# Performance work log

Hardware: AMD Instinct MI355X
Metric: run time of the kernel (lower is better)

Reference implementation:

```python
import jax, jax.numpy as jnp
import numpy as np

VOCAB = 32000
D_MODEL = 1024


def setup_inputs() -> dict:
    key = jax.random.key(0)
    k = jax.random.split(key, 8)
    B, H, T, S = 8, 16, 128, 512
    src = jax.random.randint(k[0], (B, S), 0, VOCAB)
    decode_output = jax.random.normal(k[1], (B, T, D_MODEL), dtype=jnp.float32)
    decode_attn = jax.random.uniform(k[2], (B, H, T, S), dtype=jnp.float32)
    memory = jax.random.normal(k[3], (B, S, D_MODEL), dtype=jnp.float32)
    W_gen = jax.random.normal(k[4], (VOCAB, D_MODEL), dtype=jnp.float32) * (1.0 / np.sqrt(D_MODEL))
    b_gen = jnp.zeros((VOCAB,), dtype=jnp.float32)
    W_prob = jax.random.normal(k[5], (1, 2 * D_MODEL), dtype=jnp.float32) * (1.0 / np.sqrt(2 * D_MODEL))
    b_prob = jnp.zeros((1,), dtype=jnp.float32)
    return {"src": src, "decode_output": decode_output, "decode_attn": decode_attn,
            "memory": memory, "W_gen": W_gen, "b_gen": b_gen,
            "W_prob": W_prob, "b_prob": b_prob}


def reference(src, decode_output, decode_attn, memory, W_gen, b_gen, W_prob, b_prob):
    # mean over heads: [B, T, S]
    attn = jnp.mean(decode_attn, axis=1)
    B, T, S = attn.shape
    V = W_gen.shape[0]

    # generation logits: [B, T, V]
    gen_logits = jnp.einsum('btd,vd->btv', decode_output, W_gen) + b_gen

    # context vector: [B, T, D]
    context = jnp.einsum('bts,bsd->btd', attn, memory)

    # scatter-add copy distribution over vocab: [B, T, V]
    src_exp = jnp.broadcast_to(src[:, None, :], (B, T, S))  # token ids per step
    b_idx = jnp.arange(B)[:, None, None]
    t_idx = jnp.arange(T)[None, :, None]
    copy_logits = jnp.zeros((B, T, V), dtype=attn.dtype).at[b_idx, t_idx, src_exp].add(attn)

    # copy gate: sigmoid(Linear([context; decode_output])) -> [B, T, 1]
    cat = jnp.concatenate([context, decode_output], axis=-1)
    prob = jax.nn.sigmoid(jnp.einsum('btd,od->bto', cat, W_prob) + b_prob)

    gen_p = prob * jax.nn.softmax(gen_logits, axis=-1)
    copy_p = (1.0 - prob) * jax.nn.softmax(copy_logits, axis=-1)
    final = gen_p + copy_p
    return jnp.log(final).reshape(-1, V)
```

## Files before the change

### kernel.cpp

```cpp
#include <hip/hip_runtime.h>
#include <hip/hip_bf16.h>
#include <cstddef>
#include <cstdint>

#define BB 8
#define HH 16
#define TT 128
#define SS 512
#define DD 1024
#define VV 32000
#define MM (BB * TT)

typedef float f32x4 __attribute__((ext_vector_type(4)));
typedef short short8v __attribute__((ext_vector_type(8)));
typedef unsigned short ushort8v __attribute__((ext_vector_type(8)));

__device__ __forceinline__ unsigned short f2bf(float x) {
    __hip_bfloat16 h = __float2bfloat16(x);
    return __builtin_bit_cast(unsigned short, h);
}
__device__ __forceinline__ float bf2f(unsigned short u) {
    unsigned int x = ((unsigned int)u) << 16;
    return __builtin_bit_cast(float, x);
}

__device__ __forceinline__ float wave_sum(float v) {
#pragma unroll
    for (int o = 1; o < 64; o <<= 1) v += __shfl_xor(v, o);
    return v;
}
__device__ __forceinline__ float wave_max(float v) {
#pragma unroll
    for (int o = 1; o < 64; o <<= 1) v = fmaxf(v, __shfl_xor(v, o));
    return v;
}
__device__ __forceinline__ float block_sum(float v, float* red, int tid) {
    v = wave_sum(v);
    __syncthreads();
    if ((tid & 63) == 0) red[tid >> 6] = v;
    __syncthreads();
    return red[0] + red[1] + red[2] + red[3];
}
__device__ __forceinline__ float block_max(float v, float* red, int tid) {
    v = wave_max(v);
    __syncthreads();
    if ((tid & 63) == 0) red[tid >> 6] = v;
    __syncthreads();
    return fmaxf(fmaxf(red[0], red[1]), fmaxf(red[2], red[3]));
}

__global__ void k_pm_init(int* pos_map, float* zg) {
    int i = blockIdx.x * 256 + threadIdx.x;
    if (i < BB * VV) pos_map[i] = 0x7fffffff;
    if (i < MM) zg[i] = 0.0f;
}

__global__ void k_pm_build(const int* __restrict__ src, int* pos_map) {
    int b = blockIdx.x, s = threadIdx.x;
    int tok = src[b * SS + s];
    atomicMin(&pos_map[b * VV + tok], s);
}

__global__ __launch_bounds__(256) void k_cast(const float* __restrict__ in,
                                              unsigned short* __restrict__ outp, int n8) {
    int stride = gridDim.x * 256;
    for (int i = blockIdx.x * 256 + threadIdx.x; i < n8; i += stride) {
        const float4* p = reinterpret_cast<const float4*>(in + (size_t)i * 8);
        float4 a = p[0], b = p[1];
        ushort8v u;
        u[0] = f2bf(a.x); u[1] = f2bf(a.y); u[2] = f2bf(a.z); u[3] = f2bf(a.w);
        u[4] = f2bf(b.x); u[5] = f2bf(b.y); u[6] = f2bf(b.z); u[7] = f2bf(b.w);
        *reinterpret_cast<ushort8v*>(outp + (size_t)i * 8) = u;
    }
}

__global__ __launch_bounds__(256) void k_vecdots(const float* __restrict__ memory,
                                                 const float* __restrict__ dec,
                                                 const float* __restrict__ wprob,
                                                 float* mw, float* dw) {
    int row = blockIdx.x * 4 + (threadIdx.x >> 6);
    int lane = threadIdx.x & 63;
    const float4* srcv;
    const float4* wv;
    if (row < BB * SS) {
        srcv = reinterpret_cast<const float4*>(memory + (size_t)row * DD);
        wv = reinterpret_cast<const float4*>(wprob);
    } else {
        srcv = reinterpret_cast<const float4*>(dec + (size_t)(row - BB * SS) * DD);
        wv = reinterpret_cast<const float4*>(wprob + DD);
    }
    float sum = 0.f;
#pragma unroll
    for (int k = 0; k < 4; ++k) {
        int idx = lane + 64 * k;
        float4 a = srcv[idx];
        float4 w = wv[idx];
        sum += a.x * w.x + a.y * w.y + a.z * w.z + a.w * w.w;
    }
    sum = wave_sum(sum);
    if (lane == 0) {
        if (row < BB * SS) mw[row] = sum;
        else dw[row - BB * SS] = sum;
    }
}

__global__ __launch_bounds__(256) void k_row(const float* __restrict__ dattn,
                                             const int* __restrict__ src,
                                             const int* __restrict__ pos_map,
                                             const float* __restrict__ mw,
                                             const float* __restrict__ dw,
                                             const float* __restrict__ bprob,
                                             float* __restrict__ e_vals,
                                             float* __restrict__ prob,
                                             float* __restrict__ zc,
                                             float* __restrict__ c0) {
    int bt = blockIdx.x;
    int b = bt >> 7;
    int t = bt & 127;
    int tid = threadIdx.x;
    __shared__ float a_row[SS];
    __shared__ float vals[SS];
    __shared__ float red[4];

    for (int s = tid; s < SS; s += 256) {
        const float* base = dattn + ((size_t)b * HH * TT + t) * SS + s;
        float sum = 0.f;
#pragma unroll
        for (int h = 0; h < HH; ++h) sum += base[(size_t)h * TT * SS];
        a_row[s] = sum * 0.0625f;
        vals[s] = 0.f;
    }
    __syncthreads();
    for (int s = tid; s < SS; s += 256) {
        int rep = pos_map[b * VV + src[b * SS + s]];
        atomicAdd(&vals[rep], a_row[s]);
    }
    __syncthreads();
    float psum = 0.f;
    for (int s = tid; s < SS; s += 256) psum += a_row[s] * mw[b * SS + s];
    psum = block_sum(psum, red, tid);
    float z = psum + dw[bt] + bprob[0];
    float p = 1.0f / (1.0f + __expf(-z));
    float mxv = -3.4e38f;
    for (int s = tid; s < SS; s += 256) {
        int rep = pos_map[b * VV + src[b * SS + s]];
        if (rep == s) mxv = fmaxf(mxv, vals[s]);
    }
    mxv = block_max(mxv, red, tid);
    float m_c = fmaxf(0.0f, mxv);
    float sexp = 0.f, cnt = 0.f;
    for (int s = tid; s < SS; s += 256) {
        int rep = pos_map[b * VV + src[b * SS + s]];
        float e = 0.0f;
        if (rep == s) {
            e = __expf(vals[s] - m_c);
            sexp += e;
            cnt += 1.0f;
        }
        e_vals[(size_t)bt * SS + s] = e;
    }
    sexp = block_sum(sexp, red, tid);
    cnt = block_sum(cnt, red, tid);
    if (tid == 0) {
        prob[bt] = p;
        zc[bt] = ((float)VV - cnt) * __expf(-m_c) + sexp;
        c0[bt] = __expf(-m_c);
    }
}

#define NKT 32
#define BUFE 12288

#define AS1 __attribute__((address_space(1)))
#define AS3 __attribute__((address_space(3)))

template <int EPI>
__global__ __launch_bounds__(512, 4) void k_gemm_bf(const unsigned short* __restrict__ Abf,
                                                    const unsigned short* __restrict__ Wbf,
                                                    const float* __restrict__ bgen,
                                                    float* __restrict__ out,
                                                    unsigned short* __restrict__ ebuf,
                                                    float* __restrict__ zg) {
    __shared__ unsigned short lds[3 * BUFE];

    int tid = threadIdx.x;
    int p = blockIdx.x;
    int wg = (p & 7) * 125 + (p >> 3);
    int mt = wg & 7, nt = wg >> 3;
    int m0 = mt * 128, v0 = nt * 256;

    int lane = tid & 63, w = tid >> 6;
    int wm = w & 1, wn = w >> 1;

    int srow = tid >> 2;
    int scol = (tid & 3) << 3;
    const unsigned short* gA = Abf + (size_t)(m0 + srow) * DD + scol;
    const unsigned short* gB = Wbf + (size_t)(v0 + srow) * DD + scol;

#define STAGE(T, BI) do {                                                              \
    size_t ko_ = (size_t)(T) * 32;                                                     \
    __builtin_amdgcn_global_load_lds(                                                  \
        (const AS1 void*)(gA + ko_),                                                   \
        (AS3 void*)(lds + (BI) * BUFE + tid * 8), 16, 0, 0);                           \
    __builtin_amdgcn_global_load_lds(                                                  \
        (const AS1 void*)(gB + ko_),                                                   \
        (AS3 void*)(lds + (BI) * BUFE + 4096 + tid * 8), 16, 0, 0);                    \
    __builtin_amdgcn_global_load_lds(                                                  \
        (const AS1 void*)(gB + (size_t)128 * DD + ko_),                                \
        (AS3 void*)(lds + (BI) * BUFE + 8192 + tid * 8), 16, 0, 0);                    \
} while (0)

    int lr = lane & 15, kg8 = (lane >> 4) << 3;
    const unsigned short* arow = lds + (wm * 64 + lr) * 32 + kg8;
    const unsigned short* brow = lds + 4096 + (wn * 64 + lr) * 32 + kg8;

    f32x4 acc[4][4] = {};

#define ITER(T, BI, DO_STAGE, VM)  do {                                                \
    __builtin_amdgcn_s_barrier();                                                      \
    short8v af[4], bfr[4];                                                             \
    _Pragma("unroll")                                                                  \
    for (int i = 0; i < 4; ++i)                                                        \
        af[i] = *reinterpret_cast<const short8v*>(arow + (BI) * BUFE + i * (16 * 32)); \
    _Pragma("unroll")                                                                  \
    for (int j = 0; j < 4; ++j)                                                        \
        bfr[j] = *reinterpret_cast<const short8v*>(brow + (BI) * BUFE + j * (16 * 32));\
    if (DO_STAGE) STAGE((T) + 2, ((BI) + 2) % 3);                                      \
    asm volatile("s_waitcnt lgkmcnt(0)" ::: "memory");                                 \
    __builtin_amdgcn_sched_barrier(0);                                                 \
    __builtin_amdgcn_s_setprio(1);                                                     \
    _Pragma("unroll")                                                                  \
    for (int i = 0; i < 4; ++i)                                                        \
        _Pragma("unroll")                                                              \
        for (int j = 0; j < 4; ++j)                                                    \
            acc[i][j] = __builtin_amdgcn_mfma_f32_16x16x32_bf16(af[i], bfr[j], acc[i][j], 0, 0, 0); \
    __builtin_amdgcn_s_setprio(0);                                                     \
    if ((VM) == 3) asm volatile("s_waitcnt vmcnt(3)" ::: "memory");                    \
    else if ((VM) == 0) asm volatile("s_waitcnt vmcnt(0)" ::: "memory");               \
} while (0)

    STAGE(0, 0);
    STAGE(1, 1);
    asm volatile("s_waitcnt vmcnt(3)" ::: "memory");

    for (int t = 0; t < NKT - 2; t += 3) {
        ITER(t + 0, 0, true, 3);
        ITER(t + 1, 1, true, 3);
        ITER(t + 2, 2, true, 3);
    }
    ITER(30, 0, false, 0);
    ITER(31, 1, false, -1);
#undef ITER
#undef STAGE

    int colb = lane & 15, rgrp = lane >> 4;
#pragma unroll
    for (int i = 0; i < 4; ++i) {
        float es0 = 0.f, es1 = 0.f, es2 = 0.f, es3 = 0.f;
        int gmb = m0 + wm * 64 + i * 16 + rgrp * 4;
#pragma unroll
        for (int j = 0; j < 4; ++j) {
            int gv = v0 + wn * 64 + j * 16 + colb;
            float bgj = bgen[gv];
            float v0f = acc[i][j][0] + bgj;
            float v1f = acc[i][j][1] + bgj;
            float v2f = acc[i][j][2] + bgj;
            float v3f = acc[i][j][3] + bgj;
            float e0 = __expf(v0f), e1 = __expf(v1f), e2 = __expf(v2f), e3 = __expf(v3f);
            if constexpr (EPI == 1) {
                ebuf[(size_t)(gmb + 0) * VV + gv] = f2bf(e0);
                ebuf[(size_t)(gmb + 1) * VV + gv] = f2bf(e1);
                ebuf[(size_t)(gmb + 2) * VV + gv] = f2bf(e2);
                ebuf[(size_t)(gmb + 3) * VV + gv] = f2bf(e3);
            } else {
                out[(size_t)(gmb + 0) * VV + gv] = v0f;
                out[(size_t)(gmb + 1) * VV + gv] = v1f;
                out[(size_t)(gmb + 2) * VV + gv] = v2f;
                out[(size_t)(gmb + 3) * VV + gv] = v3f;
            }
            es0 += e0; es1 += e1; es2 += e2; es3 += e3;
        }
        float es[4] = {es0, es1, es2, es3};
#pragma unroll
        for (int rr = 0; rr < 4; ++rr) {
            float e = es[rr];
            e += __shfl_xor(e, 1); e += __shfl_xor(e, 2);
            e += __shfl_xor(e, 4); e += __shfl_xor(e, 8);
            if (colb == 0) atomicAdd(&zg[gmb + rr], e);
        }
    }
}

#define FBb 128
#define FLDK 40

__global__ __launch_bounds__(256) void k_gemm_f32(const float* __restrict__ A,
                                                  const float* __restrict__ Wg,
                                                  const float* __restrict__ bgen,
                                                  float* __restrict__ out,
                                                  float* __restrict__ zg) {
    __shared__ unsigned short As[FBb * FLDK];
    __shared__ unsigned short Bs[FBb * FLDK];
    int tid = threadIdx.x;
    int bid = blockIdx.x;
    int mt = bid & 7;
    int nt = bid >> 3;
    int m0 = mt * FBb, v0 = nt * FBb;
    int lane = tid & 63, wid = tid >> 6;
    int wr = (wid >> 1) * 64, wc = (wid & 1) * 64;
    int lr = lane & 15, lk = (lane >> 4) << 3;
    int r = tid >> 1, c0 = (tid & 1) << 4;

    f32x4 acc[4][4] = {};

    for (int k0 = 0; k0 < DD; k0 += 32) {
        {
            const float4* pa = reinterpret_cast<const float4*>(A + (size_t)(m0 + r) * DD + k0 + c0);
            float4 x0 = pa[0], x1 = pa[1], x2 = pa[2], x3 = pa[3];
            ushort8v u0, u1;
            u0[0] = f2bf(x0.x); u0[1] = f2bf(x0.y); u0[2] = f2bf(x0.z); u0[3] = f2bf(x0.w);
            u0[4] = f2bf(x1.x); u0[5] = f2bf(x1.y); u0[6] = f2bf(x1.z); u0[7] = f2bf(x1.w);
            u1[0] = f2bf(x2.x); u1[1] = f2bf(x2.y); u1[2] = f2bf(x2.z); u1[3] = f2bf(x2.w);
            u1[4] = f2bf(x3.x); u1[5] = f2bf(x3.y); u1[6] = f2bf(x3.z); u1[7] = f2bf(x3.w);
            *reinterpret_cast<ushort8v*>(&As[r * FLDK + c0]) = u0;
            *reinterpret_cast<ushort8v*>(&As[r * FLDK + c0 + 8]) = u1;

            const float4* pb = reinterpret_cast<const float4*>(Wg + (size_t)(v0 + r) * DD + k0 + c0);
            float4 y0 = pb[0], y1 = pb[1], y2 = pb[2], y3 = pb[3];
            ushort8v w0, w1;
            w0[0] = f2bf(y0.x); w0[1] = f2bf(y0.y); w0[2] = f2bf(y0.z); w0[3] = f2bf(y0.w);
            w0[4] = f2bf(y1.x); w0[5] = f2bf(y1.y); w0[6] = f2bf(y1.z); w0[7] = f2bf(y1.w);
            w1[0] = f2bf(y2.x); w1[1] = f2bf(y2.y); w1[2] = f2bf(y2.z); w1[3] = f2bf(y2.w);
            w1[4] = f2bf(y3.x); w1[5] = f2bf(y3.y); w1[6] = f2bf(y3.z); w1[7] = f2bf(y3.w);
            *reinterpret_cast<ushort8v*>(&Bs[r * FLDK + c0]) = w0;
            *reinterpret_cast<ushort8v*>(&Bs[r * FLDK + c0 + 8]) = w1;
        }
        __syncthreads();

        short8v af[4], bfr[4];
#pragma unroll
        for (int i = 0; i < 4; ++i)
            af[i] = *reinterpret_cast<const short8v*>(&As[(wr + i * 16 + lr) * FLDK + lk]);
#pragma unroll
        for (int j = 0; j < 4; ++j)
            bfr[j] = *reinterpret_cast<const short8v*>(&Bs[(wc + j * 16 + lr) * FLDK + lk]);
#pragma unroll
        for (int i = 0; i < 4; ++i)
#pragma unroll
            for (int j = 0; j < 4; ++j)
                acc[i][j] = __builtin_amdgcn_mfma_f32_16x16x32_bf16(af[i], bfr[j], acc[i][j], 0, 0, 0);
        __syncthreads();
    }

    int colb = lane & 15;
    int rgrp = lane >> 4;
#pragma unroll
    for (int i = 0; i < 4; ++i) {
        float es0 = 0.f, es1 = 0.f, es2 = 0.f, es3 = 0.f;
        int gmb = m0 + wr + i * 16 + rgrp * 4;
#pragma unroll
        for (int j = 0; j < 4; ++j) {
            int gv = v0 + wc + j * 16 + colb;
            float bgj = bgen[gv];
            float v0f = acc[i][j][0] + bgj;
            float v1f = acc[i][j][1] + bgj;
            float v2f = acc[i][j][2] + bgj;
            float v3f = acc[i][j][3] + bgj;
            out[(size_t)(gmb + 0) * VV + gv] = v0f;
            out[(size_t)(gmb + 1) * VV + gv] = v1f;
            out[(size_t)(gmb + 2) * VV + gv] = v2f;
            out[(size_t)(gmb + 3) * VV + gv] = v3f;
            es0 += __expf(v0f); es1 += __expf(v1f);
            es2 += __expf(v2f); es3 += __expf(v3f);
        }
        float es[4] = {es0, es1, es2, es3};
#pragma unroll
        for (int rr = 0; rr < 4; ++rr) {
            float e = es[rr];
            e += __shfl_xor(e, 1); e += __shfl_xor(e, 2);
            e += __shfl_xor(e, 4); e += __shfl_xor(e, 8);
            if (colb == 0) atomicAdd(&zg[gmb + rr], e);
        }
    }
}

template <int RD16>
__global__ __launch_bounds__(256) void k_final(float* __restrict__ gen,
                                               const unsigned short* __restrict__ ebuf,
                                               const int* __restrict__ pos_map,
                                               const float* __restrict__ e_vals,
                                               const float* __restrict__ prob,
                                               const float* __restrict__ zc,
                                               const float* __restrict__ c0,
                                               const float* __restrict__ zg) {
    int m = blockIdx.x;
    int b = m >> 7;
    int tid = threadIdx.x;
    float p = prob[m];
    float A1 = p / zg[m];
    float A2 = (1.0f - p) / zc[m];
    float cc = c0[m];
    const float* ev = e_vals + (size_t)m * SS;
    float4* row = reinterpret_cast<float4*>(gen + (size_t)m * VV);
    const int4* pm = reinterpret_cast<const int4*>(pos_map + b * VV);
    if constexpr (RD16 == 1) {
        const ushort8v* erow = reinterpret_cast<const ushort8v*>(ebuf + (size_t)m * VV);
        for (int i = tid; i < VV / 8; i += 256) {
            ushort8v ee = erow[i];
            int4 rp0 = pm[2 * i], rp1 = pm[2 * i + 1];
            float4 o0, o1;
            o0.x = __logf(A1 * bf2f(ee[0]) + A2 * ((rp0.x < SS) ? ev[rp0.x] : cc));
            o0.y = __logf(A1 * bf2f(ee[1]) + A2 * ((rp0.y < SS) ? ev[rp0.y] : cc));
            o0.z = __logf(A1 * bf2f(ee[2]) + A2 * ((rp0.z < SS) ? ev[rp0.z] : cc));
            o0.w = __logf(A1 * bf2f(ee[3]) + A2 * ((rp0.w < SS) ? ev[rp0.w] : cc));
            o1.x = __logf(A1 * bf2f(ee[4]) + A2 * ((rp1.x < SS) ? ev[rp1.x] : cc));
            o1.y = __logf(A1 * bf2f(ee[5]) + A2 * ((rp1.y < SS) ? ev[rp1.y] : cc));
            o1.z = __logf(A1 * bf2f(ee[6]) + A2 * ((rp1.z < SS) ? ev[rp1.z] : cc));
            o1.w = __logf(A1 * bf2f(ee[7]) + A2 * ((rp1.w < SS) ? ev[rp1.w] : cc));
            row[2 * i] = o0;
            row[2 * i + 1] = o1;
        }
    } else {
        for (int i = tid; i < VV / 4; i += 256) {
            float4 g = row[i];
            int4 rp = pm[i];
            float4 o;
            o.x = __logf(A1 * __expf(g.x) + A2 * ((rp.x < SS) ? ev[rp.x] : cc));
            o.y = __logf(A1 * __expf(g.y) + A2 * ((rp.y < SS) ? ev[rp.y] : cc));
            o.z = __logf(A1 * __expf(g.z) + A2 * ((rp.z < SS) ? ev[rp.z] : cc));
            o.w = __logf(A1 * __expf(g.w) + A2 * ((rp.w < SS) ? ev[rp.w] : cc));
            row[i] = o;
        }
    }
}

extern "C" void kernel_launch(void* const* d_in, const int* in_sizes, int n_in,
                              void* d_out, int out_size, void* d_ws, size_t ws_size,
                              hipStream_t stream) {
    const int* src = (const int*)d_in[0];
    const float* dec = (const float*)d_in[1];
    const float* dattn = (const float*)d_in[2];
    const float* mem = (const float*)d_in[3];
    const float* wgen = (const float*)d_in[4];
    const float* bgen = (const float*)d_in[5];
    const float* wprob = (const float*)d_in[6];
    const float* bprob = (const float*)d_in[7];
    float* out = (float*)d_out;
    char* ws = (char*)d_ws;

    int* pos_map = (int*)(ws + 0);
    float* e_vals = (float*)(ws + 1048576);
    float* mw   = (float*)(ws + 3145728);
    float* dw   = (float*)(ws + 3145728 + 16384);
    float* prob = (float*)(ws + 3145728 + 20480);
    float* zc   = (float*)(ws + 3145728 + 24576);
    float* c0   = (float*)(ws + 3145728 + 28672);
    float* zg   = (float*)(ws + 3145728 + 32768);
    unsigned short* Wbf = (unsigned short*)(ws + 3211264);
    unsigned short* Abf = (unsigned short*)(ws + 3211264 + 65536000);
    unsigned short* Ebf = (unsigned short*)(ws + 3211264 + 65536000 + 2097152);
    const size_t NEEDED  = 3211264ull + 65536000ull + 2097152ull;
    const size_t NEEDED2 = NEEDED + 65536000ull;

    k_pm_init<<<(BB * VV + 255) / 256, 256, 0, stream>>>(pos_map, zg);
    k_pm_build<<<BB, SS, 0, stream>>>(src, pos_map);
    k_vecdots<<<(BB * SS + MM) / 4, 256, 0, stream>>>(mem, dec, wprob, mw, dw);
    k_row<<<MM, 256, 0, stream>>>(dattn, src, pos_map, mw, dw, bprob, e_vals, prob, zc, c0);

    if (ws_size >= NEEDED) {
        k_cast<<<2048, 256, 0, stream>>>(wgen, Wbf, VV * DD / 8);
        k_cast<<<512, 256, 0, stream>>>(dec, Abf, MM * DD / 8);
        if (ws_size >= NEEDED2) {
            k_gemm_bf<1><<<(MM / 128) * (VV / 256), 512, 0, stream>>>(Abf, Wbf, bgen, out, Ebf, zg);
            k_final<1><<<MM, 256, 0, stream>>>(out, Ebf, pos_map, e_vals, prob, zc, c0, zg);
        } else {
            k_gemm_bf<0><<<(MM / 128) * (VV / 256), 512, 0, stream>>>(Abf, Wbf, bgen, out, Ebf, zg);
            k_final<0><<<MM, 256, 0, stream>>>(out, Ebf, pos_map, e_vals, prob, zc, c0, zg);
        }
    } else {
        k_gemm_f32<<<(MM / FBb) * (VV / FBb), 256, 0, stream>>>(dec, wgen, bgen, out, zg);
        k_final<0><<<MM, 256, 0, stream>>>(out, Ebf, pos_map, e_vals, prob, zc, c0, zg);
    }
}
```

Baseline: 222.9 us.

## Fuse fp32-to-bf16 cast of W_gen into GEMM B-tile staging with LDS swizzle

Drops the separate kernel that cast the 131 MB fp32 W_gen to bf16 in workspace. The GEMM now loads fp32 weights into registers, converts them to bf16 and writes them into XOR-swizzled LDS. The A tile keeps its async global-to-LDS path, using a matching swizzle to cut bank conflicts. This removes a full read-write pass over the weights, but the GEMM now reads twice the weight bytes and is re-read across the 8 M tiles. The register-staged pipeline also adds VALU conversion work and extra waits.

```diff
diff --git a/kernel.cpp b/kernel.cpp
--- a/kernel.cpp
+++ b/kernel.cpp
@@ -176,7 +176,7 @@
 
 template <int EPI>
 __global__ __launch_bounds__(512, 4) void k_gemm_bf(const unsigned short* __restrict__ Abf,
-                                                    const unsigned short* __restrict__ Wbf,
+                                                    const float* __restrict__ Wg,
                                                     const float* __restrict__ bgen,
                                                     float* __restrict__ out,
                                                     unsigned short* __restrict__ ebuf,
@@ -185,47 +185,65 @@
 
     int tid = threadIdx.x;
     int p = blockIdx.x;
-    int wg = (p & 7) * 125 + (p >> 3);
-    int mt = wg & 7, nt = wg >> 3;
+    int wgid = (p & 7) * 125 + (p >> 3);
+    int mt = wgid & 7, nt = wgid >> 3;
     int m0 = mt * 128, v0 = nt * 256;
 
     int lane = tid & 63, w = tid >> 6;
     int wm = w & 1, wn = w >> 1;
 
-    int srow = tid >> 2;
-    int scol = (tid & 3) << 3;
-    const unsigned short* gA = Abf + (size_t)(m0 + srow) * DD + scol;
-    const unsigned short* gB = Wbf + (size_t)(v0 + srow) * DD + scol;
-
-#define STAGE(T, BI) do {                                                              \
-    size_t ko_ = (size_t)(T) * 32;                                                     \
-    __builtin_amdgcn_global_load_lds(                                                  \
-        (const AS1 void*)(gA + ko_),                                                   \
-        (AS3 void*)(lds + (BI) * BUFE + tid * 8), 16, 0, 0);                           \
-    __builtin_amdgcn_global_load_lds(                                                  \
-        (const AS1 void*)(gB + ko_),                                                   \
-        (AS3 void*)(lds + (BI) * BUFE + 4096 + tid * 8), 16, 0, 0);                    \
-    __builtin_amdgcn_global_load_lds(                                                  \
-        (const AS1 void*)(gB + (size_t)128 * DD + ko_),                                \
-        (AS3 void*)(lds + (BI) * BUFE + 8192 + tid * 8), 16, 0, 0);                    \
-} while (0)
-
-    int lr = lane & 15, kg8 = (lane >> 4) << 3;
-    const unsigned short* arow = lds + (wm * 64 + lr) * 32 + kg8;
-    const unsigned short* brow = lds + 4096 + (wn * 64 + lr) * 32 + kg8;
+    int srowA = tid >> 2;
+    int schA = (tid & 3) ^ ((tid >> 3) & 3);
+    const unsigned short* gA = Abf + (size_t)(m0 + srowA) * DD + schA * 8;
+
+    int browB = tid >> 1;
+    int bhalf = tid & 1;
+    const float* gB = Wg + (size_t)(v0 + browB) * DD + bhalf * 16;
+    int xw = (tid >> 2) & 3;
+    unsigned short* wB0 = lds + 4096 + browB * 32 + ((((bhalf << 1) | 0) ^ xw) << 3);
+    unsigned short* wB1 = lds + 4096 + browB * 32 + ((((bhalf << 1) | 1) ^ xw) << 3);
+
+    float4 br0, br1, br2, br3;
+
+#define LOADB(T) do { size_t ko_ = (size_t)(T) * 32;                                   \
+    br0 = *reinterpret_cast<const float4*>(gB + ko_);                                  \
+    br1 = *reinterpret_cast<const float4*>(gB + ko_ + 4);                              \
+    br2 = *reinterpret_cast<const float4*>(gB + ko_ + 8);                              \
+    br3 = *reinterpret_cast<const float4*>(gB + ko_ + 12); } while (0)
+
+#define STAGEA(T, BI) __builtin_amdgcn_global_load_lds(                                \
+    (const AS1 void*)(gA + (size_t)(T) * 32),                                          \
+    (AS3 void*)(lds + (BI) * BUFE + tid * 8), 16, 0, 0)
+
+#define WRITEB(BI) do {                                                                \
+    ushort8v bw0_, bw1_;                                                               \
+    bw0_[0] = f2bf(br0.x); bw0_[1] = f2bf(br0.y); bw0_[2] = f2bf(br0.z); bw0_[3] = f2bf(br0.w); \
+    bw0_[4] = f2bf(br1.x); bw0_[5] = f2bf(br1.y); bw0_[6] = f2bf(br1.z); bw0_[7] = f2bf(br1.w); \
+    bw1_[0] = f2bf(br2.x); bw1_[1] = f2bf(br2.y); bw1_[2] = f2bf(br2.z); bw1_[3] = f2bf(br2.w); \
+    bw1_[4] = f2bf(br3.x); bw1_[5] = f2bf(br3.y); bw1_[6] = f2bf(br3.z); bw1_[7] = f2bf(br3.w); \
+    *reinterpret_cast<ushort8v*>(wB0 + (BI) * BUFE) = bw0_;                            \
+    *reinterpret_cast<ushort8v*>(wB1 + (BI) * BUFE) = bw1_; } while (0)
+
+    int lr = lane & 15, kg = lane >> 4;
+    int xr = (lr >> 1) & 3;
+    const unsigned short* arow = lds + (wm * 64 + lr) * 32 + ((kg ^ xr) << 3);
+    const unsigned short* brow = lds + 4096 + (wn * 64 + lr) * 32 + ((kg ^ xr) << 3);
 
     f32x4 acc[4][4] = {};
 
-#define ITER(T, BI, DO_STAGE, VM)  do {                                                \
-    __builtin_amdgcn_s_barrier();                                                      \
+#define ITER(T, BI, MODE) do {                                                         \
     short8v af[4], bfr[4];                                                             \
     _Pragma("unroll")                                                                  \
     for (int i = 0; i < 4; ++i)                                                        \
-        af[i] = *reinterpret_cast<const short8v*>(arow + (BI) * BUFE + i * (16 * 32)); \
+        af[i] = *reinterpret_cast<const short8v*>(arow + (BI) * BUFE + i * 512);       \
     _Pragma("unroll")                                                                  \
     for (int j = 0; j < 4; ++j)                                                        \
-        bfr[j] = *reinterpret_cast<const short8v*>(brow + (BI) * BUFE + j * (16 * 32));\
-    if (DO_STAGE) STAGE((T) + 2, ((BI) + 2) % 3);                                      \
+        bfr[j] = *reinterpret_cast<const short8v*>(brow + (BI) * BUFE + j * 512);      \
+    if ((MODE) >= 1) {                                                                 \
+        asm volatile("s_waitcnt vmcnt(1)" ::: "memory");                               \
+        WRITEB(((BI) + 1) % 3);                                                        \
+    }                                                                                  \
+    if ((MODE) == 2) { LOADB((T) + 2); STAGEA((T) + 2, ((BI) + 2) % 3); }              \
     asm volatile("s_waitcnt lgkmcnt(0)" ::: "memory");                                 \
     __builtin_amdgcn_sched_barrier(0);                                                 \
     __builtin_amdgcn_s_setprio(1);                                                     \
@@ -235,23 +253,31 @@
         for (int j = 0; j < 4; ++j)                                                    \
             acc[i][j] = __builtin_amdgcn_mfma_f32_16x16x32_bf16(af[i], bfr[j], acc[i][j], 0, 0, 0); \
     __builtin_amdgcn_s_setprio(0);                                                     \
-    if ((VM) == 3) asm volatile("s_waitcnt vmcnt(3)" ::: "memory");                    \
-    else if ((VM) == 0) asm volatile("s_waitcnt vmcnt(0)" ::: "memory");               \
+    if ((MODE) == 2) asm volatile("s_waitcnt vmcnt(5)" ::: "memory");                  \
+    else if ((MODE) == 1) asm volatile("s_waitcnt vmcnt(0)" ::: "memory");             \
+    if ((MODE) >= 1) __builtin_amdgcn_s_barrier();                                     \
 } while (0)
 
-    STAGE(0, 0);
-    STAGE(1, 1);
-    asm volatile("s_waitcnt vmcnt(3)" ::: "memory");
+    LOADB(0);
+    STAGEA(0, 0);
+    asm volatile("s_waitcnt vmcnt(1)" ::: "memory");
+    WRITEB(0);
+    LOADB(1);
+    STAGEA(1, 1);
+    asm volatile("s_waitcnt vmcnt(5)" ::: "memory");
+    __builtin_amdgcn_s_barrier();
 
     for (int t = 0; t < NKT - 2; t += 3) {
-        ITER(t + 0, 0, true, 3);
-        ITER(t + 1, 1, true, 3);
-        ITER(t + 2, 2, true, 3);
-    }
-    ITER(30, 0, false, 0);
-    ITER(31, 1, false, -1);
+        ITER(t + 0, 0, 2);
+        ITER(t + 1, 1, 2);
+        ITER(t + 2, 2, 2);
+    }
+    ITER(30, 0, 1);
+    ITER(31, 1, 0);
 #undef ITER
-#undef STAGE
+#undef WRITEB
+#undef STAGEA
+#undef LOADB
 
     int colb = lane & 15, rgrp = lane >> 4;
 #pragma unroll
@@ -456,10 +482,9 @@
     float* zc   = (float*)(ws + 3145728 + 24576);
     float* c0   = (float*)(ws + 3145728 + 28672);
     float* zg   = (float*)(ws + 3145728 + 32768);
-    unsigned short* Wbf = (unsigned short*)(ws + 3211264);
-    unsigned short* Abf = (unsigned short*)(ws + 3211264 + 65536000);
-    unsigned short* Ebf = (unsigned short*)(ws + 3211264 + 65536000 + 2097152);
-    const size_t NEEDED  = 3211264ull + 65536000ull + 2097152ull;
+    unsigned short* Abf = (unsigned short*)(ws + 3211264);
+    unsigned short* Ebf = (unsigned short*)(ws + 3211264 + 2097152);
+    const size_t NEEDED  = 3211264ull + 2097152ull;
     const size_t NEEDED2 = NEEDED + 65536000ull;
 
     k_pm_init<<<(BB * VV + 255) / 256, 256, 0, stream>>>(pos_map, zg);
@@ -468,13 +493,12 @@
     k_row<<<MM, 256, 0, stream>>>(dattn, src, pos_map, mw, dw, bprob, e_vals, prob, zc, c0);
 
     if (ws_size >= NEEDED) {
-        k_cast<<<2048, 256, 0, stream>>>(wgen, Wbf, VV * DD / 8);
         k_cast<<<512, 256, 0, stream>>>(dec, Abf, MM * DD / 8);
         if (ws_size >= NEEDED2) {
-            k_gemm_bf<1><<<(MM / 128) * (VV / 256), 512, 0, stream>>>(Abf, Wbf, bgen, out, Ebf, zg);
+            k_gemm_bf<1><<<(MM / 128) * (VV / 256), 512, 0, stream>>>(Abf, wgen, bgen, out, Ebf, zg);
             k_final<1><<<MM, 256, 0, stream>>>(out, Ebf, pos_map, e_vals, prob, zc, c0, zg);
         } else {
-            k_gemm_bf<0><<<(MM / 128) * (VV / 256), 512, 0, stream>>>(Abf, Wbf, bgen, out, Ebf, zg);
+            k_gemm_bf<0><<<(MM / 128) * (VV / 256), 512, 0, stream>>>(Abf, wgen, bgen, out, Ebf, zg);
             k_final<0><<<MM, 256, 0, stream>>>(out, Ebf, pos_map, e_vals, prob, zc, c0, zg);
         }
     } else {
```

New measurement: 499.2 us. 124% more time.
